# Kernel optimization log

Measured on AMD Instinct MI355X. Metric: run time of the kernel, lower is better.

Reference implementation:

```python
import jax, jax.numpy as jnp
import numpy as np

BS, SL, NN, NE = 8, 100, 200, 600
C = 110; CP1 = C + 1
D = 128          # node_embed_dim
DC = 64          # concept_embed_dim
H = 256          # lstm hidden
VOCAB = 50000
NPROB = 1000
FEAT = 2 + CP1 + DC  # LSTM input dim = 177


def setup_inputs() -> dict:
    key = jax.random.key(0)
    ks = jax.random.split(key, 24)
    f32 = jnp.float32
    p_id = jax.random.randint(ks[0], (BS, SL), 0, NPROB)
    c_id = jax.random.bernoulli(ks[1], 0.1, (BS, SL, CP1)).astype(f32)
    node_id = jax.random.randint(ks[2], (BS, SL, NN), 0, VOCAB)
    edge = jax.random.randint(ks[3], (BS, SL, 2, NE), 0, NN)
    edge_type = jax.random.randint(ks[4], (BS, SL, NE), 0, 8)
    target_c = jax.random.bernoulli(ks[5], 0.05, (BS, SL, CP1)).astype(f32)
    target_c = target_c.at[:, :, 0].set(1.0)  # every step has >=1 target concept
    result = jax.random.bernoulli(ks[6], 0.5, (BS * SL, 1)).astype(f32)
    c_embed = jax.random.bernoulli(ks[7], 0.1, (BS, SL, CP1)).astype(f32)
    cur_result = jax.random.normal(ks[8], (BS, SL, 2), f32)
    # parameters
    node_embed_w = jax.random.normal(ks[9], (VOCAB, D), f32) * 0.02
    edge_embed_w = (jax.random.normal(ks[10], (8, D), f32) * 0.02).at[0].set(0.0)  # padding_idx=0
    ggnn_w = jax.random.normal(ks[11], (4, D, D), f32) * 0.05
    gru_w_ih = jax.random.normal(ks[12], (3 * D, D), f32) * 0.05
    gru_w_hh = jax.random.normal(ks[13], (3 * D, D), f32) * 0.05
    gru_b_ih = jnp.zeros((3 * D,), f32)
    gru_b_hh = jnp.zeros((3 * D,), f32)
    transdim_w = jax.random.normal(ks[14], (DC, D), f32) * 0.05
    concept_embedding = jax.random.normal(ks[15], (CP1, DC), f32) * 0.05
    lstm_w_ih = jax.random.normal(ks[16], (4 * H, FEAT), f32) * 0.05
    lstm_w_hh = jax.random.normal(ks[17], (4 * H, H), f32) * 0.05
    lstm_b_ih = jnp.zeros((4 * H,), f32)
    lstm_b_hh = jnp.zeros((4 * H,), f32)
    pred_w = jax.random.normal(ks[18], (CP1, H), f32) * 0.05
    pred_b = jnp.zeros((CP1,), f32)
    return dict(p_id=p_id, c_id=c_id, node_id=node_id, edge=edge, edge_type=edge_type,
                target_c=target_c, result=result, c_embed=c_embed, cur_result=cur_result,
                node_embed_w=node_embed_w, edge_embed_w=edge_embed_w, ggnn_w=ggnn_w,
                gru_w_ih=gru_w_ih, gru_w_hh=gru_w_hh, gru_b_ih=gru_b_ih, gru_b_hh=gru_b_hh,
                transdim_w=transdim_w, concept_embedding=concept_embedding,
                lstm_w_ih=lstm_w_ih, lstm_w_hh=lstm_w_hh, lstm_b_ih=lstm_b_ih,
                lstm_b_hh=lstm_b_hh, pred_w=pred_w, pred_b=pred_b)


def _forward(p_id, c_id, node_id, edge, edge_type, target_c, result, c_embed, cur_result,
             node_embed_w, edge_embed_w, ggnn_w, gru_w_ih, gru_w_hh, gru_b_ih, gru_b_hh,
             transdim_w, concept_embedding, lstm_w_ih, lstm_w_hh, lstm_b_ih, lstm_b_hh,
             pred_w, pred_b):
    bs, sl = p_id.shape
    N = node_id.shape[2]
    G = bs * sl  # all graphs batched (replaces torch per-sample python loop)
    x = node_embed_w[node_id].reshape(G, N, -1)                       # [G,N,D]
    ew = edge_embed_w[edge_type].mean(-1).reshape(G, -1, 1)           # [G,E,1]
    e = edge.reshape(G, 2, -1)
    src, dst = e[:, 0], e[:, 1]                                       # [G,E]
    flat_dst = (dst + jnp.arange(G)[:, None] * N).reshape(-1)
    d = x.shape[-1]
    # GatedGraphConv, 4 layers: m = x @ W_l, sum-aggregate edge_weight*m[src] at dst, GRUCell update
    for l in range(4):
        m = jnp.einsum('gnd,de->gne', x, ggnn_w[l])
        gathered = jnp.take_along_axis(m, src[:, :, None], axis=1)    # [G,E,D]
        msg = (ew * gathered).reshape(-1, d)
        agg = jax.ops.segment_sum(msg, flat_dst, num_segments=G * N).reshape(G, N, d)
        gi = agg @ gru_w_ih.T + gru_b_ih
        gh = x @ gru_w_hh.T + gru_b_hh
        i_r, i_z, i_n = jnp.split(gi, 3, axis=-1)
        h_r, h_z, h_n = jnp.split(gh, 3, axis=-1)
        r = jax.nn.sigmoid(i_r + h_r)
        z = jax.nn.sigmoid(i_z + h_z)
        n = jnp.tanh(i_n + r * h_n)
        x = (1.0 - z) * n + z * x
    # transdim (node_embed_dim != concept_embed_dim)
    ggnn = jnp.einsum('gnd,cd->gnc', x, transdim_w)                   # [G,N,DC]
    # concept-node attention
    ce = c_embed.reshape(G, -1, 1)                                    # [G,C+1,1]
    query = ce * concept_embedding[None]                              # [G,C+1,DC]
    attn_w = jax.nn.softmax(jnp.einsum('gcd,gnd->gcn', query, ggnn), axis=2)
    attn = jnp.einsum('gcn,gnd->gcd', attn_w, ggnn) * ce
    num = jnp.sum(c_id, axis=2).reshape(G, 1)
    num = jnp.where(num == 0, 1.0, num)
    attn_out = (jnp.sum(attn, axis=1) / num).reshape(bs, sl, -1)
    # LSTM (1 layer, batch_first)
    lstm_in = jnp.concatenate([c_embed, attn_out, cur_result], axis=2)
    hdim = pred_w.shape[1]
    def step(carry, xt):
        h, c = carry
        gates = xt @ lstm_w_ih.T + lstm_b_ih + h @ lstm_w_hh.T + lstm_b_hh
        i, f, g, o = jnp.split(gates, 4, axis=-1)
        c = jax.nn.sigmoid(f) * c + jax.nn.sigmoid(i) * jnp.tanh(g)
        h = jax.nn.sigmoid(o) * jnp.tanh(c)
        return (h, c), h
    init = (jnp.zeros((bs, hdim), lstm_in.dtype), jnp.zeros((bs, hdim), lstm_in.dtype))
    _, hs = jax.lax.scan(step, init, jnp.swapaxes(lstm_in, 0, 1))
    lstm_out = jnp.swapaxes(hs, 0, 1).reshape(G, hdim)
    # prediction + masked BCE-with-logits
    pred = lstm_out @ pred_w.T + pred_b                               # [G,C+1]
    tc = target_c.reshape(G, -1)
    pred1 = jnp.sum(pred * tc, axis=1)
    nc = jnp.sum(tc, axis=1)
    mask = nc > 0
    fp = pred1 / jnp.where(mask, nc, 1.0)
    ft = result.reshape(-1)
    bce = jnp.maximum(fp, 0.0) - fp * ft + jnp.log1p(jnp.exp(-jnp.abs(fp)))
    mf = mask.astype(fp.dtype)
    loss = jnp.sum(bce * mf) / jnp.maximum(jnp.sum(mf), 1.0)
    return loss, jax.nn.sigmoid(fp), ft


def reference(p_id, c_id, node_id, edge, edge_type, target_c, result, c_embed, cur_result,
              node_embed_w, edge_embed_w, ggnn_w, gru_w_ih, gru_w_hh, gru_b_ih, gru_b_hh,
              transdim_w, concept_embedding, lstm_w_ih, lstm_w_hh, lstm_b_ih, lstm_b_hh,
              pred_w, pred_b):
    return _forward(p_id, c_id, node_id, edge, edge_type, target_c, result, c_embed, cur_result,
                    node_embed_w, edge_embed_w, ggnn_w, gru_w_ih, gru_w_hh, gru_b_ih, gru_b_hh,
                    transdim_w, concept_embedding, lstm_w_ih, lstm_w_hh, lstm_b_ih, lstm_b_hh,
                    pred_w, pred_b)
```

## Files before the change

kernel.cpp:

```cpp
#include <hip/hip_runtime.h>
#include <math.h>

static const int BSZ   = 8;
static const int SLN   = 100;
static const int NNODE = 200;
static const int NEDGE = 600;
static const int CP1N  = 111;
static const int DIM   = 128;
static const int DCN   = 64;
static const int HID   = 256;
static const int FEATN = 177;
static const int GN    = 800;
static const int MROW  = 160000;

typedef unsigned short u16;
typedef u16    u16x8  __attribute__((ext_vector_type(8)));
typedef __bf16 bf16x8 __attribute__((ext_vector_type(8)));
typedef __bf16 bf16x2 __attribute__((ext_vector_type(2)));
typedef float  f32x16 __attribute__((ext_vector_type(16)));

#if defined(__has_builtin)
# if __has_builtin(__builtin_amdgcn_fdot2_f32_bf16)
#  define HAVE_FDOT2 1
# else
#  define HAVE_FDOT2 0
# endif
#else
# define HAVE_FDOT2 0
#endif

__device__ __forceinline__ float sigf(float v){ return 1.0f/(1.0f + expf(-v)); }
__device__ __forceinline__ u16 f2bf(float f){
    union { float f; unsigned u; } v; v.f = f;
    unsigned r = v.u + 0x7FFFu + ((v.u >> 16) & 1u);
    return (u16)(r >> 16);
}
__device__ __forceinline__ float bf2f(u16 u){
    union { unsigned u; float f; } v; v.u = ((unsigned)u) << 16;
    return v.f;
}
__device__ __forceinline__ float dot2bf(unsigned w, unsigned h, float acc){
#if HAVE_FDOT2
    return __builtin_amdgcn_fdot2_f32_bf16(__builtin_bit_cast(bf16x2, w),
                                           __builtin_bit_cast(bf16x2, h), acc, false);
#else
    acc += bf2f((u16)(w & 0xffffu)) * bf2f((u16)(h & 0xffffu));
    acc += bf2f((u16)(w >> 16))     * bf2f((u16)(h >> 16));
    return acc;
#endif
}

__global__ void k_transpose_w(const float* __restrict__ whh, const float* __restrict__ wih,
                              unsigned* __restrict__ whhP, float* __restrict__ wihT){
    int idx = blockIdx.x*blockDim.x + threadIdx.x;
    const int total1 = 128*1024;
    if (idx < total1){
        int k2 = idx >> 10, j = idx & 1023;
        u16 lo = f2bf(whh[(size_t)j*256 + 2*k2]);
        u16 hi = f2bf(whh[(size_t)j*256 + 2*k2 + 1]);
        whhP[(size_t)k2*1024 + j] = (unsigned)lo | ((unsigned)hi << 16);
    }
    int idx2 = idx - total1;
    const int total2 = FEATN*1024;
    if (idx2 >= 0 && idx2 < total2){
        int k = idx2 >> 10, j = idx2 & 1023;
        wihT[(size_t)k*1024 + j] = wih[(size_t)j*FEATN + k];
    }
}

__global__ void k_convert_w(const float* __restrict__ wih, const float* __restrict__ whh,
                            const float* __restrict__ gw, const float* __restrict__ tw,
                            u16* __restrict__ wihb, u16* __restrict__ whhb,
                            u16* __restrict__ gwTb, u16* __restrict__ twb){
    int idx = blockIdx.x*blockDim.x + threadIdx.x;
    if (idx < 49152){
        wihb[idx] = f2bf(wih[idx]);
    } else if (idx < 98304){
        int t = idx - 49152;
        whhb[t] = f2bf(whh[t]);
    } else if (idx < 163840){
        int t = idx - 98304;
        int l = t >> 14, rem = t & 16383, n = rem >> 7, k = rem & 127;
        gwTb[t] = f2bf(gw[((size_t)l*128 + k)*128 + n]);
    } else if (idx < 172032){
        int t = idx - 163840;
        twb[t] = f2bf(tw[t]);
    }
}

__global__ void __launch_bounds__(256)
k_build_csr(const int* __restrict__ edge, const int* __restrict__ etype,
            const float* __restrict__ eembed,
            int* __restrict__ csr_src, float* __restrict__ csr_w, int* __restrict__ csr_off){
    int g = blockIdx.x; int tid = threadIdx.x;
    __shared__ float tmean[8];
    __shared__ float tpart[8][32];
    __shared__ int cnt[NNODE];
    __shared__ int offs[NNODE+1];
    __shared__ int cur[NNODE];
    {
        int ty = tid >> 5, lane = tid & 31;
        float s = 0.f;
        for (int i = lane; i < DIM; i += 32) s += eembed[ty*DIM + i];
        tpart[ty][lane] = s;
    }
    for (int i = tid; i < NNODE; i += 256) cnt[i] = 0;
    __syncthreads();
    if (tid < 8){
        float s = 0.f;
        for (int i = 0; i < 32; i++) s += tpart[tid][i];
        tmean[tid] = s / (float)DIM;
    }
    for (int e = tid; e < NEDGE; e += 256){
        int dst = edge[((size_t)g*2+1)*NEDGE + e];
        atomicAdd(&cnt[dst], 1);
    }
    __syncthreads();
    if (tid == 0){
        int run = 0;
        for (int i = 0; i < NNODE; i++){ offs[i] = run; run += cnt[i]; }
        offs[NNODE] = run;
    }
    __syncthreads();
    for (int i = tid; i < NNODE; i += 256) cur[i] = offs[i];
    for (int i = tid; i < NNODE+1; i += 256) csr_off[(size_t)g*(NNODE+1)+i] = offs[i];
    __syncthreads();
    for (int e = tid; e < NEDGE; e += 256){
        int dst = edge[((size_t)g*2+1)*NEDGE + e];
        int src = edge[((size_t)g*2+0)*NEDGE + e];
        float w = tmean[etype[(size_t)g*NEDGE + e]];
        int pos = atomicAdd(&cur[dst], 1);
        csr_src[(size_t)g*NEDGE + pos] = src;
        csr_w [(size_t)g*NEDGE + pos] = w;
    }
}

__global__ void k_gather_x(const int* __restrict__ nid, const float4* __restrict__ emb,
                           u16x8* __restrict__ xb){
    const long total = (long)MROW*16;
    for (long c = (long)blockIdx.x*blockDim.x + threadIdx.x; c < total; c += (long)gridDim.x*blockDim.x){
        long row = c >> 4; int p = (int)(c & 15);
        float4 a = emb[(size_t)nid[row]*32 + p*2];
        float4 b = emb[(size_t)nid[row]*32 + p*2 + 1];
        u16x8 v;
        v[0]=f2bf(a.x); v[1]=f2bf(a.y); v[2]=f2bf(a.z); v[3]=f2bf(a.w);
        v[4]=f2bf(b.x); v[5]=f2bf(b.y); v[6]=f2bf(b.z); v[7]=f2bf(b.w);
        xb[c] = v;
    }
}

__global__ void __launch_bounds__(256)
k_mm_scatter(const u16* __restrict__ xb, const u16* __restrict__ gwTb_l,
             const int* __restrict__ csr_src, const float* __restrict__ csr_w,
             const int* __restrict__ csr_off, u16* __restrict__ aggb){
    __shared__ u16 smem[224*128];
    __shared__ int   e_src[NEDGE];
    __shared__ float e_w[NEDGE];
    __shared__ int   offs_s[NNODE+1];
    int g = blockIdx.x;
    int tid = threadIdx.x;
    const u16x8* xg = (const u16x8*)(xb + (size_t)g*NNODE*DIM);
    u16x8* afrag = (u16x8*)smem;
    for (int c = tid; c < 3584; c += 256){
        int row = c >> 4, kc8 = c & 15;
        u16x8 v = {};
        if (row < NNODE) v = xg[row*16 + kc8];
        afrag[((row>>5)*8 + (kc8>>1))*64 + (row&31) + 32*(kc8&1)] = v;
    }
    {
        const int*   srcp = csr_src + (size_t)g*NEDGE;
        const float* wp   = csr_w   + (size_t)g*NEDGE;
        const int*   off  = csr_off + (size_t)g*(NNODE+1);
        for (int i = tid; i < NEDGE; i += 256){ e_src[i] = srcp[i]; e_w[i] = wp[i]; }
        for (int i = tid; i <= NNODE; i += 256) offs_s[i] = off[i];
    }
    __syncthreads();
    int w = tid >> 6, lane = tid & 63;
    int nbase = w*32;
    int m = lane & 31, kh = lane >> 5;
    f32x16 acc[7];
    #pragma unroll
    for (int t = 0; t < 7; t++) acc[t] = (f32x16)0.f;
    const u16x8* bp = (const u16x8*)gwTb_l;
    int nrow = nbase + m;
    #pragma unroll
    for (int kc = 0; kc < 8; kc++){
        u16x8 b = bp[nrow*16 + kc*2 + kh];
        #pragma unroll
        for (int mt = 0; mt < 7; mt++){
            u16x8 a = afrag[(mt*8 + kc)*64 + lane];
            acc[mt] = __builtin_amdgcn_mfma_f32_32x32x16_bf16(
                __builtin_bit_cast(bf16x8, a), __builtin_bit_cast(bf16x8, b), acc[mt], 0, 0, 0);
        }
    }
    __syncthreads();
    #pragma unroll
    for (int mt = 0; mt < 7; mt++){
        #pragma unroll
        for (int r = 0; r < 16; r++){
            int row = mt*32 + (r&3) + 8*(r>>2) + 4*kh;
            int col = nbase + m;
            smem[row*128 + col] = f2bf(acc[mt][r]);
        }
    }
    __syncthreads();
    const unsigned* m32 = (const unsigned*)smem;
    int j2 = tid & 63, rg = tid >> 6;
    unsigned* aggout = (unsigned*)(aggb + (size_t)g*NNODE*DIM);
    for (int i = 0; i < 50; i++){
        int n = rg*50 + i;
        int b0 = offs_s[n], e0 = offs_s[n+1];
        float a0 = 0.f, a1 = 0.f;
        for (int p = b0; p < e0; p++){
            unsigned mv = m32[e_src[p]*64 + j2];
            float w_ = e_w[p];
            a0 += w_ * bf2f((u16)(mv & 0xffffu));
            a1 += w_ * bf2f((u16)(mv >> 16));
        }
        aggout[(size_t)n*64 + j2] = (unsigned)f2bf(a0) | ((unsigned)f2bf(a1) << 16);
    }
}

__global__ void __launch_bounds__(512, 2)
k_gru_mfma(u16* __restrict__ xb, const u16* __restrict__ aggb,
           const u16* __restrict__ wihb, const u16* __restrict__ whhb,
           const float* __restrict__ bih, const float* __restrict__ bhh){
    __shared__ u16x8 afragA[2048];
    __shared__ u16x8 afragX[2048];
    int tid = threadIdx.x;
    long r0 = (long)blockIdx.x * 128;
    const u16x8* aggp = (const u16x8*)aggb;
    const u16x8* xbp  = (const u16x8*)xb;
    for (int c = tid; c < 4096; c += 512){
        int mat = c >> 11, cc = c & 2047;
        int row = cc >> 4, kc8 = cc & 15;
        u16x8 v = (mat ? xbp : aggp)[(r0 + row)*16 + kc8];
        int slot = ((row>>5)*8 + (kc8>>1))*64 + (row&31) + 32*(kc8&1);
        (mat ? afragX : afragA)[slot] = v;
    }
    __syncthreads();
    int w = tid >> 6, lane = tid & 63;
    int mtg = w >> 2;
    int cb  = (w & 3) * 32;
    f32x16 acc0[6], acc1[6];
    #pragma unroll
    for (int t = 0; t < 6; t++){ acc0[t] = (f32x16)0.f; acc1[t] = (f32x16)0.f; }
    const u16x8* bi = (const u16x8*)wihb;
    const u16x8* bh = (const u16x8*)whhb;
    int kh = lane >> 5;
    int ncol = cb + (lane & 31);
    #pragma unroll
    for (int kc = 0; kc < 8; kc++){
        u16x8 aA0 = afragA[((2*mtg+0)*8 + kc)*64 + lane];
        u16x8 aA1 = afragA[((2*mtg+1)*8 + kc)*64 + lane];
        u16x8 aX0 = afragX[((2*mtg+0)*8 + kc)*64 + lane];
        u16x8 aX1 = afragX[((2*mtg+1)*8 + kc)*64 + lane];
        #pragma unroll
        for (int g3 = 0; g3 < 3; g3++){
            int n = g3*128 + ncol;
            u16x8 b1 = bi[n*16 + kc*2 + kh];
            u16x8 b2 = bh[n*16 + kc*2 + kh];
            acc0[g3]   = __builtin_amdgcn_mfma_f32_32x32x16_bf16(
                __builtin_bit_cast(bf16x8, aA0), __builtin_bit_cast(bf16x8, b1), acc0[g3], 0,0,0);
            acc1[g3]   = __builtin_amdgcn_mfma_f32_32x32x16_bf16(
                __builtin_bit_cast(bf16x8, aA1), __builtin_bit_cast(bf16x8, b1), acc1[g3], 0,0,0);
            acc0[3+g3] = __builtin_amdgcn_mfma_f32_32x32x16_bf16(
                __builtin_bit_cast(bf16x8, aX0), __builtin_bit_cast(bf16x8, b2), acc0[3+g3], 0,0,0);
            acc1[3+g3] = __builtin_amdgcn_mfma_f32_32x32x16_bf16(
                __builtin_bit_cast(bf16x8, aX1), __builtin_bit_cast(bf16x8, b2), acc1[3+g3], 0,0,0);
        }
    }
    int col = cb + (lane & 31);
    float bir = bih[col], biz = bih[col+128], bin = bih[col+256];
    float bhr = bhh[col], bhz = bhh[col+128], bhn = bhh[col+256];
    int kc8c = col >> 3, elc = col & 7;
    #pragma unroll
    for (int mt2 = 0; mt2 < 2; mt2++){
        const f32x16* ac = mt2 ? acc1 : acc0;
        #pragma unroll
        for (int r = 0; r < 16; r++){
            int row = mtg*64 + mt2*32 + (r&3) + 8*(r>>2) + 4*kh;
            u16x8 xv = afragX[((row>>5)*8 + (kc8c>>1))*64 + (row&31) + 32*(kc8c&1)];
            float xo = bf2f(((const u16*)&xv)[elc]);
            float rr  = sigf(ac[0][r] + bir + ac[3][r] + bhr);
            float zz  = sigf(ac[1][r] + biz + ac[4][r] + bhz);
            float nn_ = tanhf(ac[2][r] + bin + rr*(ac[5][r] + bhn));
            float xn  = (1.f - zz)*nn_ + zz*xo;
            xb[(size_t)(r0 + row)*DIM + col] = f2bf(xn);
        }
    }
}

__global__ void __launch_bounds__(256)
k_transdim(const u16* __restrict__ xb, const u16* __restrict__ twb, float* __restrict__ out){
    int tid = threadIdx.x;
    int w = tid >> 6, lane = tid & 63;
    int m = lane & 31, kh = lane >> 5;
    long r0 = (long)blockIdx.x * 128;
    const u16x8* xp = (const u16x8*)xb;
    const u16x8* tp = (const u16x8*)twb;
    long rowA = r0 + w*32 + m;
    f32x16 acc[2];
    acc[0] = (f32x16)0.f; acc[1] = (f32x16)0.f;
    #pragma unroll
    for (int kc = 0; kc < 8; kc++){
        u16x8 a = xp[rowA*16 + kc*2 + kh];
        #pragma unroll
        for (int nt = 0; nt < 2; nt++){
            u16x8 b = tp[(nt*32 + m)*16 + kc*2 + kh];
            acc[nt] = __builtin_amdgcn_mfma_f32_32x32x16_bf16(
                __builtin_bit_cast(bf16x8, a), __builtin_bit_cast(bf16x8, b), acc[nt], 0,0,0);
        }
    }
    #pragma unroll
    for (int nt = 0; nt < 2; nt++){
        #pragma unroll
        for (int r = 0; r < 16; r++){
            int row = w*32 + (r&3) + 8*(r>>2) + 4*kh;
            int col = nt*32 + m;
            out[(r0 + row)*DCN + col] = acc[nt][r];
        }
    }
}

__global__ void __launch_bounds__(256)
k_attention(const float* __restrict__ gout, const float* __restrict__ cemb,
            const float* __restrict__ cid, const float* __restrict__ conc,
            const float* __restrict__ curres, float* __restrict__ lstm_in){
    int g = blockIdx.x; int tid = threadIdx.x;
    __shared__ float gg[NNODE*65];
    __shared__ float ce_s[CP1N];
    __shared__ float q_s[DCN];
    __shared__ float sc[256];
    __shared__ float red[256];
    __shared__ float part[4][DCN];
    __shared__ float oacc[DCN];
    __shared__ float num_s;
    if (tid < CP1N) ce_s[tid] = cemb[(size_t)g*CP1N + tid];
    if (tid < DCN) oacc[tid] = 0.f;
    for (int i = tid; i < NNODE*DCN; i += 256){
        int n = i >> 6, d = i & 63;
        gg[n*65 + d] = gout[((size_t)g*NNODE + n)*DCN + d];
    }
    red[tid] = (tid < CP1N) ? cid[(size_t)g*CP1N + tid] : 0.f;
    __syncthreads();
    for (int s = 128; s > 0; s >>= 1){ if (tid < s) red[tid] += red[tid+s]; __syncthreads(); }
    if (tid == 0){ float nm = red[0]; num_s = (nm == 0.f) ? 1.f : nm; }
    __syncthreads();
    for (int c = 0; c < CP1N; c++){
        float ce = ce_s[c];
        if (ce == 0.f) continue;
        if (tid < DCN) q_s[tid] = ce * conc[c*DCN + tid];
        __syncthreads();
        float s = 0.f;
        if (tid < NNODE){
            const float* gr_ = &gg[tid*65];
            #pragma unroll 16
            for (int d = 0; d < DCN; d++) s += q_s[d] * gr_[d];
        }
        red[tid] = (tid < NNODE) ? s : -1e30f;
        __syncthreads();
        for (int t2 = 128; t2 > 0; t2 >>= 1){ if (tid < t2) red[tid] = fmaxf(red[tid], red[tid+t2]); __syncthreads(); }
        float mx = red[0];
        __syncthreads();
        float e = (tid < NNODE) ? expf(s - mx) : 0.f;
        sc[tid] = e;
        red[tid] = e;
        __syncthreads();
        for (int t2 = 128; t2 > 0; t2 >>= 1){ if (tid < t2) red[tid] += red[tid+t2]; __syncthreads(); }
        float inv = ce / red[0];
        int d = tid & 63, ngp = tid >> 6;
        float pa = 0.f;
        for (int n = ngp; n < NNODE; n += 4) pa += sc[n] * gg[n*65 + d];
        part[ngp][d] = pa;
        __syncthreads();
        if (tid < DCN) oacc[tid] += inv * (part[0][tid] + part[1][tid] + part[2][tid] + part[3][tid]);
        __syncthreads();
    }
    if (tid < FEATN){
        float v;
        if      (tid < CP1N)       v = ce_s[tid];
        else if (tid < CP1N+DCN)   v = oacc[tid-CP1N] / num_s;
        else                       v = curres[(size_t)g*2 + (tid-CP1N-DCN)];
        lstm_in[(size_t)g*FEATN + tid] = v;
    }
}

__global__ void __launch_bounds__(256)
k_gi(const float* __restrict__ lstm_in, const float* __restrict__ wihT,
     const float* __restrict__ bih, const float* __restrict__ bhh, float* __restrict__ gi){
    int rb = blockIdx.x;
    int jb = blockIdx.y;
    int tid = threadIdx.x;
    __shared__ float in_s[8][FEATN];
    for (int i = tid; i < 8*FEATN; i += 256){ int r = i/FEATN, k = i%FEATN; in_s[r][k] = lstm_in[((size_t)rb*8+r)*FEATN + k]; }
    __syncthreads();
    int j = jb*256 + tid;
    float acc[8];
    #pragma unroll
    for (int i = 0; i < 8; i++) acc[i] = 0.f;
    for (int k = 0; k < FEATN; k++){
        float w = wihT[(size_t)k*1024 + j];
        #pragma unroll
        for (int i = 0; i < 8; i++) acc[i] += in_s[i][k] * w;
    }
    float b = bih[j] + bhh[j];
    #pragma unroll
    for (int i = 0; i < 8; i++) gi[((size_t)rb*8+i)*1024 + j] = acc[i] + b;
}

static const int WREG = 104;
static const int WL4  = 6;

__global__ void __launch_bounds__(1024)
__attribute__((amdgpu_waves_per_eu(4,4)))
k_lstm(const float* __restrict__ gi, const unsigned* __restrict__ whhP, float* __restrict__ out){
    int b = blockIdx.x; int tid = threadIdx.x;
    __shared__ uint4 ldsw4[WL4][1024];
    __shared__ float gates[1024];
    __shared__ __align__(8) u16 h16[HID];
    unsigned wreg[WREG];
    #pragma unroll
    for (int i = 0; i < WREG; i++) wreg[i] = whhP[(size_t)i*1024 + tid];
    #pragma unroll
    for (int q = 0; q < WL4; q++){
        uint4 v;
        v.x = whhP[(size_t)(WREG + 4*q + 0)*1024 + tid];
        v.y = whhP[(size_t)(WREG + 4*q + 1)*1024 + tid];
        v.z = whhP[(size_t)(WREG + 4*q + 2)*1024 + tid];
        v.w = whhP[(size_t)(WREG + 4*q + 3)*1024 + tid];
        ldsw4[q][tid] = v;
    }
    if (tid < 128) ((unsigned*)h16)[tid] = 0u;
    float c_reg = 0.f;
    int lane = tid & 63;
    __syncthreads();
    float giv = gi[(size_t)b*SLN*1024 + tid];
    for (int t = 0; t < SLN; t++){
        unsigned hv0 = ((const unsigned*)h16)[lane];
        unsigned hv1 = ((const unsigned*)h16)[64 + lane];
        float acc0 = giv, acc1 = 0.f;
        if (t+1 < SLN) giv = gi[((size_t)b*SLN + t + 1)*1024 + tid];
        #pragma unroll
        for (int p = 0; p < 64; p += 2){
            unsigned hpa = (unsigned)__builtin_amdgcn_readlane((int)hv0, p);
            unsigned hpb = (unsigned)__builtin_amdgcn_readlane((int)hv0, p+1);
            acc0 = dot2bf(wreg[p],   hpa, acc0);
            acc1 = dot2bf(wreg[p+1], hpb, acc1);
        }
        #pragma unroll
        for (int p = 64; p < WREG; p += 2){
            unsigned hpa = (unsigned)__builtin_amdgcn_readlane((int)hv1, p - 64);
            unsigned hpb = (unsigned)__builtin_amdgcn_readlane((int)hv1, p - 63);
            acc0 = dot2bf(wreg[p],   hpa, acc0);
            acc1 = dot2bf(wreg[p+1], hpb, acc1);
        }
        #pragma unroll
        for (int q = 0; q < WL4; q++){
            uint4 wv = ldsw4[q][tid];
            int base = WREG + 4*q - 64;
            unsigned h0 = (unsigned)__builtin_amdgcn_readlane((int)hv1, base + 0);
            unsigned h1 = (unsigned)__builtin_amdgcn_readlane((int)hv1, base + 1);
            unsigned h2 = (unsigned)__builtin_amdgcn_readlane((int)hv1, base + 2);
            unsigned h3 = (unsigned)__builtin_amdgcn_readlane((int)hv1, base + 3);
            acc0 = dot2bf(wv.x, h0, acc0);
            acc1 = dot2bf(wv.y, h1, acc1);
            acc0 = dot2bf(wv.z, h2, acc0);
            acc1 = dot2bf(wv.w, h3, acc1);
        }
        gates[tid] = acc0 + acc1;
        __syncthreads();
        if (tid < HID){
            float i_ = sigf(gates[tid]);
            float f_ = sigf(gates[tid+256]);
            float g_ = tanhf(gates[tid+512]);
            float o_ = sigf(gates[tid+768]);
            c_reg = f_*c_reg + i_*g_;
            float h = o_*tanhf(c_reg);
            out[((size_t)b*SLN + t)*HID + tid] = h;
            h16[tid] = f2bf(h);
        }
        __syncthreads();
    }
}

__global__ void __launch_bounds__(128)
k_final(const float* __restrict__ lstm_out, const float* __restrict__ pw, const float* __restrict__ pb,
        const float* __restrict__ tc, const float* __restrict__ result,
        float* __restrict__ out, float* __restrict__ lacc){
    int row = blockIdx.x; int tid = threadIdx.x;
    __shared__ __align__(16) float h_s[HID];
    __shared__ float redv[128], redn[128];
    h_s[tid]       = lstm_out[(size_t)row*HID + tid];
    h_s[tid + 128] = lstm_out[(size_t)row*HID + tid + 128];
    __syncthreads();
    float v = 0.f, n = 0.f;
    if (tid < CP1N){
        float acc = pb[tid];
        const float4* wr = (const float4*)(pw + (size_t)tid*HID);
        const float4* hp = (const float4*)h_s;
        #pragma unroll 8
        for (int k4 = 0; k4 < 64; k4++){
            float4 w = wr[k4]; float4 h4 = hp[k4];
            acc += h4.x*w.x + h4.y*w.y + h4.z*w.z + h4.w*w.w;
        }
        float t = tc[(size_t)row*CP1N + tid];
        v = acc*t; n = t;
    }
    redv[tid] = v; redn[tid] = n;
    __syncthreads();
    for (int s = 64; s > 0; s >>= 1){
        if (tid < s){ redv[tid] += redv[tid+s]; redn[tid] += redn[tid+s]; }
        __syncthreads();
    }
    if (tid == 0){
        float nc = redn[0];
        bool mask = nc > 0.f;
        float fp = redv[0] / (mask ? nc : 1.f);
        float ft = result[row];
        float bce = fmaxf(fp, 0.f) - fp*ft + log1pf(expf(-fabsf(fp)));
        out[1 + row]      = 1.f/(1.f + expf(-fp));
        out[1 + GN + row] = ft;
        if (mask){ atomicAdd(&lacc[0], bce); atomicAdd(&lacc[1], 1.f); }
    }
}

__global__ void k_loss_final(const float* __restrict__ lacc, float* __restrict__ out){
    out[0] = lacc[0] / fmaxf(lacc[1], 1.f);
}

extern "C" void kernel_launch(void* const* d_in, const int* in_sizes, int n_in,
                              void* d_out, int out_size, void* d_ws, size_t ws_size,
                              hipStream_t stream) {
    const float* c_id        = (const float*)d_in[1];
    const int*   node_id     = (const int*)  d_in[2];
    const int*   edge        = (const int*)  d_in[3];
    const int*   etype       = (const int*)  d_in[4];
    const float* target_c    = (const float*)d_in[5];
    const float* result      = (const float*)d_in[6];
    const float* c_embed     = (const float*)d_in[7];
    const float* cur_result  = (const float*)d_in[8];
    const float* node_emb_w  = (const float*)d_in[9];
    const float* edge_emb_w  = (const float*)d_in[10];
    const float* ggnn_w      = (const float*)d_in[11];
    const float* gru_w_ih    = (const float*)d_in[12];
    const float* gru_w_hh    = (const float*)d_in[13];
    const float* gru_b_ih    = (const float*)d_in[14];
    const float* gru_b_hh    = (const float*)d_in[15];
    const float* transdim_w  = (const float*)d_in[16];
    const float* concept     = (const float*)d_in[17];
    const float* lstm_w_ih   = (const float*)d_in[18];
    const float* lstm_w_hh   = (const float*)d_in[19];
    const float* lstm_b_ih   = (const float*)d_in[20];
    const float* lstm_b_hh   = (const float*)d_in[21];
    const float* pred_w      = (const float*)d_in[22];
    const float* pred_b      = (const float*)d_in[23];
    float* out = (float*)d_out;

    char* ws = (char*)d_ws;
    size_t off = 0;
    auto alloc = [&](size_t bytes) -> void* {
        void* p = ws + off;
        off += (bytes + 255) & ~(size_t)255;
        return p;
    };
    u16*      xb       = (u16*)     alloc((size_t)MROW*DIM*2);
    u16*      aggb     = (u16*)     alloc((size_t)MROW*DIM*2);
    int*      csr_src  = (int*)     alloc((size_t)GN*NEDGE*4);
    float*    csr_w    = (float*)   alloc((size_t)GN*NEDGE*4);
    int*      csr_off  = (int*)     alloc((size_t)GN*(NNODE+1)*4);
    float*    lstm_in  = (float*)   alloc((size_t)GN*FEATN*4);
    float*    gi       = (float*)   alloc((size_t)GN*1024*4);
    unsigned* whhP     = (unsigned*)alloc((size_t)128*1024*4);
    float*    wihT     = (float*)   alloc((size_t)FEATN*1024*4);
    float*    lstm_out = (float*)   alloc((size_t)GN*HID*4);
    u16*      wihb     = (u16*)     alloc((size_t)384*128*2);
    u16*      whhb     = (u16*)     alloc((size_t)384*128*2);
    u16*      gwTb     = (u16*)     alloc((size_t)4*128*128*2);
    u16*      twb      = (u16*)     alloc((size_t)DCN*DIM*2);
    float*    lacc     = (float*)   alloc(256);
    float*    ggnn_out = (float*)aggb;

    hipMemsetAsync(lacc, 0, 8, stream);
    {
        int total = 128*1024 + FEATN*1024;
        k_transpose_w<<<(total + 255)/256, 256, 0, stream>>>(lstm_w_hh, lstm_w_ih, whhP, wihT);
    }
    k_convert_w<<<672, 256, 0, stream>>>(gru_w_ih, gru_w_hh, ggnn_w, transdim_w, wihb, whhb, gwTb, twb);
    k_build_csr<<<GN, 256, 0, stream>>>(edge, etype, edge_emb_w, csr_src, csr_w, csr_off);
    k_gather_x<<<4096, 256, 0, stream>>>(node_id, (const float4*)node_emb_w, (u16x8*)xb);
    for (int l = 0; l < 4; l++){
        k_mm_scatter<<<GN, 256, 0, stream>>>(xb, gwTb + (size_t)l*DIM*DIM,
                                             csr_src, csr_w, csr_off, aggb);
        k_gru_mfma<<<MROW/128, 512, 0, stream>>>(xb, aggb, wihb, whhb, gru_b_ih, gru_b_hh);
    }
    k_transdim<<<MROW/128, 256, 0, stream>>>(xb, twb, ggnn_out);
    k_attention<<<GN, 256, 0, stream>>>(ggnn_out, c_embed, c_id, concept, cur_result, lstm_in);
    k_gi<<<dim3(100, 4), 256, 0, stream>>>(lstm_in, wihT, lstm_b_ih, lstm_b_hh, gi);
    k_lstm<<<BSZ, 1024, 0, stream>>>(gi, whhP, lstm_out);
    k_final<<<GN, 128, 0, stream>>>(lstm_out, pred_w, pred_b, target_c, result, out, lacc);
    k_loss_final<<<1, 1, 0, stream>>>(lacc, out);
}
```

Before: 1.323 ms.

## Interleave LSTM gate layout to drop a barrier; bf16 transdim output; shuffle reductions

The recurrent weights and input-gate projections are permuted so that the four gates of each hidden unit sit in adjacent lanes. Each LSTM step can then combine gates with width-4 shuffles and double-buffer h in LDS, which removes one block barrier and the shared gates array from every sequential step. The attention kernel replaces its tree reductions in shared memory with wave shuffles, and the concept-attention input is stored in bf16 to halve its traffic. The cost is lower precision in the attention input and some redundant gate math across the four lanes of each group.

```diff
diff --git a/kernel.cpp b/kernel.cpp
--- a/kernel.cpp
+++ b/kernel.cpp
@@ -55,10 +55,11 @@
     int idx = blockIdx.x*blockDim.x + threadIdx.x;
     const int total1 = 128*1024;
     if (idx < total1){
-        int k2 = idx >> 10, j = idx & 1023;
-        u16 lo = f2bf(whh[(size_t)j*256 + 2*k2]);
-        u16 hi = f2bf(whh[(size_t)j*256 + 2*k2 + 1]);
-        whhP[(size_t)k2*1024 + j] = (unsigned)lo | ((unsigned)hi << 16);
+        int k2 = idx >> 10, p = idx & 1023;
+        int jq = (p & 3)*256 + (p >> 2);
+        u16 lo = f2bf(whh[(size_t)jq*256 + 2*k2]);
+        u16 hi = f2bf(whh[(size_t)jq*256 + 2*k2 + 1]);
+        whhP[(size_t)k2*1024 + p] = (unsigned)lo | ((unsigned)hi << 16);
     }
     int idx2 = idx - total1;
     const int total2 = FEATN*1024;
@@ -292,7 +293,7 @@
 }
 
 __global__ void __launch_bounds__(256)
-k_transdim(const u16* __restrict__ xb, const u16* __restrict__ twb, float* __restrict__ out){
+k_transdim(const u16* __restrict__ xb, const u16* __restrict__ twb, u16* __restrict__ out){
     int tid = threadIdx.x;
     int w = tid >> 6, lane = tid & 63;
     int m = lane & 31, kh = lane >> 5;
@@ -318,21 +319,22 @@
         for (int r = 0; r < 16; r++){
             int row = w*32 + (r&3) + 8*(r>>2) + 4*kh;
             int col = nt*32 + m;
-            out[(r0 + row)*DCN + col] = acc[nt][r];
+            out[(r0 + row)*DCN + col] = f2bf(acc[nt][r]);
         }
     }
 }
 
 __global__ void __launch_bounds__(256)
-k_attention(const float* __restrict__ gout, const float* __restrict__ cemb,
+k_attention(const u16* __restrict__ gout, const float* __restrict__ cemb,
             const float* __restrict__ cid, const float* __restrict__ conc,
             const float* __restrict__ curres, float* __restrict__ lstm_in){
     int g = blockIdx.x; int tid = threadIdx.x;
+    int lane = tid & 63, wv = tid >> 6;
     __shared__ float gg[NNODE*65];
     __shared__ float ce_s[CP1N];
-    __shared__ float q_s[DCN];
     __shared__ float sc[256];
-    __shared__ float red[256];
+    __shared__ float wredA[4];
+    __shared__ float wredB[4];
     __shared__ float part[4][DCN];
     __shared__ float oacc[DCN];
     __shared__ float num_s;
@@ -340,43 +342,53 @@
     if (tid < DCN) oacc[tid] = 0.f;
     for (int i = tid; i < NNODE*DCN; i += 256){
         int n = i >> 6, d = i & 63;
-        gg[n*65 + d] = gout[((size_t)g*NNODE + n)*DCN + d];
-    }
-    red[tid] = (tid < CP1N) ? cid[(size_t)g*CP1N + tid] : 0.f;
-    __syncthreads();
-    for (int s = 128; s > 0; s >>= 1){ if (tid < s) red[tid] += red[tid+s]; __syncthreads(); }
-    if (tid == 0){ float nm = red[0]; num_s = (nm == 0.f) ? 1.f : nm; }
+        gg[n*65 + d] = bf2f(gout[(size_t)g*NNODE*DCN + i]);
+    }
+    {
+        float v = (tid < CP1N) ? cid[(size_t)g*CP1N + tid] : 0.f;
+        #pragma unroll
+        for (int m2 = 32; m2; m2 >>= 1) v += __shfl_xor(v, m2);
+        if (lane == 0) wredA[wv] = v;
+    }
+    __syncthreads();
+    if (tid == 0){
+        float nm = wredA[0]+wredA[1]+wredA[2]+wredA[3];
+        num_s = (nm == 0.f) ? 1.f : nm;
+    }
     __syncthreads();
     for (int c = 0; c < CP1N; c++){
         float ce = ce_s[c];
         if (ce == 0.f) continue;
-        if (tid < DCN) q_s[tid] = ce * conc[c*DCN + tid];
-        __syncthreads();
-        float s = 0.f;
+        const float* qc = conc + c*DCN;
+        float s = -1e30f;
         if (tid < NNODE){
+            float a_ = 0.f;
             const float* gr_ = &gg[tid*65];
             #pragma unroll 16
-            for (int d = 0; d < DCN; d++) s += q_s[d] * gr_[d];
-        }
-        red[tid] = (tid < NNODE) ? s : -1e30f;
+            for (int d = 0; d < DCN; d++) a_ += qc[d] * gr_[d];
+            s = ce * a_;
+        }
+        float m_ = s;
+        #pragma unroll
+        for (int m2 = 32; m2; m2 >>= 1) m_ = fmaxf(m_, __shfl_xor(m_, m2));
+        if (lane == 0) wredA[wv] = m_;
         __syncthreads();
-        for (int t2 = 128; t2 > 0; t2 >>= 1){ if (tid < t2) red[tid] = fmaxf(red[tid], red[tid+t2]); __syncthreads(); }
-        float mx = red[0];
-        __syncthreads();
+        float mx = fmaxf(fmaxf(wredA[0], wredA[1]), fmaxf(wredA[2], wredA[3]));
         float e = (tid < NNODE) ? expf(s - mx) : 0.f;
         sc[tid] = e;
-        red[tid] = e;
+        float sum_ = e;
+        #pragma unroll
+        for (int m2 = 32; m2; m2 >>= 1) sum_ += __shfl_xor(sum_, m2);
+        if (lane == 0) wredB[wv] = sum_;
         __syncthreads();
-        for (int t2 = 128; t2 > 0; t2 >>= 1){ if (tid < t2) red[tid] += red[tid+t2]; __syncthreads(); }
-        float inv = ce / red[0];
-        int d = tid & 63, ngp = tid >> 6;
+        float inv = ce / (wredB[0]+wredB[1]+wredB[2]+wredB[3]);
         float pa = 0.f;
-        for (int n = ngp; n < NNODE; n += 4) pa += sc[n] * gg[n*65 + d];
-        part[ngp][d] = pa;
+        for (int n = wv; n < NNODE; n += 4) pa += sc[n] * gg[n*65 + lane];
+        part[wv][lane] = pa;
         __syncthreads();
         if (tid < DCN) oacc[tid] += inv * (part[0][tid] + part[1][tid] + part[2][tid] + part[3][tid]);
-        __syncthreads();
-    }
+    }
+    __syncthreads();
     if (tid < FEATN){
         float v;
         if      (tid < CP1N)       v = ce_s[tid];
@@ -405,8 +417,9 @@
         for (int i = 0; i < 8; i++) acc[i] += in_s[i][k] * w;
     }
     float b = bih[j] + bhh[j];
-    #pragma unroll
-    for (int i = 0; i < 8; i++) gi[((size_t)rb*8+i)*1024 + j] = acc[i] + b;
+    int jp = (j & 255)*4 + (j >> 8);
+    #pragma unroll
+    for (int i = 0; i < 8; i++) gi[((size_t)rb*8+i)*1024 + jp] = acc[i] + b;
 }
 
 static const int WREG = 104;
@@ -417,8 +430,7 @@
 k_lstm(const float* __restrict__ gi, const unsigned* __restrict__ whhP, float* __restrict__ out){
     int b = blockIdx.x; int tid = threadIdx.x;
     __shared__ uint4 ldsw4[WL4][1024];
-    __shared__ float gates[1024];
-    __shared__ __align__(8) u16 h16[HID];
+    __shared__ unsigned hbuf[2][128];
     unsigned wreg[WREG];
     #pragma unroll
     for (int i = 0; i < WREG; i++) wreg[i] = whhP[(size_t)i*1024 + tid];
@@ -431,14 +443,15 @@
         v.w = whhP[(size_t)(WREG + 4*q + 3)*1024 + tid];
         ldsw4[q][tid] = v;
     }
-    if (tid < 128) ((unsigned*)h16)[tid] = 0u;
+    if (tid < 128) hbuf[0][tid] = 0u;
     float c_reg = 0.f;
     int lane = tid & 63;
-    __syncthreads();
+    int hq = tid >> 2;
+    __syncthreads();
+    unsigned hv0 = hbuf[0][lane];
+    unsigned hv1 = hbuf[0][64 + lane];
     float giv = gi[(size_t)b*SLN*1024 + tid];
     for (int t = 0; t < SLN; t++){
-        unsigned hv0 = ((const unsigned*)h16)[lane];
-        unsigned hv1 = ((const unsigned*)h16)[64 + lane];
         float acc0 = giv, acc1 = 0.f;
         if (t+1 < SLN) giv = gi[((size_t)b*SLN + t + 1)*1024 + tid];
         #pragma unroll
@@ -468,19 +481,25 @@
             acc0 = dot2bf(wv.z, h2, acc0);
             acc1 = dot2bf(wv.w, h3, acc1);
         }
-        gates[tid] = acc0 + acc1;
+        float gval = acc0 + acc1;
+        float v0 = __shfl(gval, 0, 4);
+        float v1 = __shfl(gval, 1, 4);
+        float v2 = __shfl(gval, 2, 4);
+        float v3 = __shfl(gval, 3, 4);
+        float i_ = sigf(v0);
+        float f_ = sigf(v1);
+        float g_ = tanhf(v2);
+        float o_ = sigf(v3);
+        c_reg = f_*c_reg + i_*g_;
+        float h = o_*tanhf(c_reg);
+        int nb = (t+1) & 1;
+        if ((tid & 3) == 0){
+            out[((size_t)b*SLN + t)*HID + hq] = h;
+            ((u16*)hbuf[nb])[hq] = f2bf(h);
+        }
         __syncthreads();
-        if (tid < HID){
-            float i_ = sigf(gates[tid]);
-            float f_ = sigf(gates[tid+256]);
-            float g_ = tanhf(gates[tid+512]);
-            float o_ = sigf(gates[tid+768]);
-            c_reg = f_*c_reg + i_*g_;
-            float h = o_*tanhf(c_reg);
-            out[((size_t)b*SLN + t)*HID + tid] = h;
-            h16[tid] = f2bf(h);
-        }
-        __syncthreads();
+        hv0 = hbuf[nb][lane];
+        hv1 = hbuf[nb][64 + lane];
     }
 }
 
@@ -579,7 +598,7 @@
     u16*      gwTb     = (u16*)     alloc((size_t)4*128*128*2);
     u16*      twb      = (u16*)     alloc((size_t)DCN*DIM*2);
     float*    lacc     = (float*)   alloc(256);
-    float*    ggnn_out = (float*)aggb;
+    u16*      ggnn_out = (u16*)aggb;
 
     hipMemsetAsync(lacc, 0, 8, stream);
     {
```

Result: slower. 1.363 ms (+3.0%).
